# Optimization experiments

Hardware: AMD Instinct MI355X
Metric: run time of the kernel (lower is better)

The kernel has to match this reference:

```python
import jax, jax.numpy as jnp
import numpy as np


def setup_inputs() -> dict:
    key = jax.random.key(0)
    k1, k2 = jax.random.split(key)
    N = 16777216  # 16M 2D points
    preds = jax.random.normal(k1, (N, 2), dtype=jnp.float32)
    targets = jax.random.normal(k2, (N, 2), dtype=jnp.float32)
    return {"preds": preds, "targets": targets}


def reference(preds, targets):
    # per-sample 2D euclidean distance, fused in one pass
    d = preds - targets                      # [N, 2]
    dist = jnp.sqrt(jnp.sum(d * d, axis=1))  # [N]
    n = dist.shape[0]
    # Faithful to torch: loss tensor starts as zeros(1) and distances are
    # cat'ed on, so mean is over n+1 elements (including a leading zero).
    loss = jnp.sum(dist) / jnp.asarray(n + 1, dist.dtype)
    return loss
```

## Files before the change

### kernel.cpp

```cpp
#include <hip/hip_runtime.h>


typedef float floatx4 __attribute__((ext_vector_type(4)));

#define NBLOCKS 4096
#define NTHREADS 256
#define UNROLL 8

__global__ __launch_bounds__(NTHREADS, 2)
void dist_partial_kernel(const floatx4* __restrict__ preds,
                         const floatx4* __restrict__ targets,
                         float* __restrict__ partials,
                         int n4) {
    const int tile_base = blockIdx.x * (UNROLL * NTHREADS) + threadIdx.x;

    float acc = 0.0f;

    if (tile_base + (UNROLL - 1) * NTHREADS < n4) {
        floatx4 p[UNROLL], t[UNROLL];
        #pragma unroll
        for (int k = 0; k < UNROLL; ++k)
            p[k] = __builtin_nontemporal_load(&preds[tile_base + k * NTHREADS]);
        #pragma unroll
        for (int k = 0; k < UNROLL; ++k)
            t[k] = __builtin_nontemporal_load(&targets[tile_base + k * NTHREADS]);
        asm volatile("" ::: "memory");
        #pragma unroll
        for (int k = 0; k < UNROLL; ++k) {
            float dx0 = p[k].x - t[k].x;
            float dy0 = p[k].y - t[k].y;
            float dx1 = p[k].z - t[k].z;
            float dy1 = p[k].w - t[k].w;
            acc += sqrtf(dx0 * dx0 + dy0 * dy0);
            acc += sqrtf(dx1 * dx1 + dy1 * dy1);
        }
    } else {
        for (int k = 0; k < UNROLL; ++k) {
            int i = tile_base + k * NTHREADS;
            if (i < n4) {
                floatx4 p = preds[i];
                floatx4 t = targets[i];
                float dx0 = p.x - t.x;
                float dy0 = p.y - t.y;
                float dx1 = p.z - t.z;
                float dy1 = p.w - t.w;
                acc += sqrtf(dx0 * dx0 + dy0 * dy0);
                acc += sqrtf(dx1 * dx1 + dy1 * dy1);
            }
        }
    }

    #pragma unroll
    for (int off = 32; off > 0; off >>= 1)
        acc += __shfl_down(acc, off, 64);

    __shared__ float wave_sums[NTHREADS / 64];
    int lane = threadIdx.x & 63;
    int wave = threadIdx.x >> 6;
    if (lane == 0) wave_sums[wave] = acc;
    __syncthreads();

    if (threadIdx.x == 0) {
        float s = 0.0f;
        #pragma unroll
        for (int w = 0; w < NTHREADS / 64; ++w) s += wave_sums[w];
        partials[blockIdx.x] = s;
    }
}

__global__ __launch_bounds__(1024)
void dist_final_kernel(const float* __restrict__ partials,
                       float* __restrict__ out,
                       int nblocks, float inv_np1) {
    int tid = threadIdx.x;
    float acc = 0.0f;
    for (int i = tid; i < nblocks; i += 1024) acc += partials[i];

    #pragma unroll
    for (int off = 32; off > 0; off >>= 1)
        acc += __shfl_down(acc, off, 64);

    __shared__ float wave_sums[16];
    int lane = tid & 63;
    int wave = tid >> 6;
    if (lane == 0) wave_sums[wave] = acc;
    __syncthreads();

    if (tid == 0) {
        float s = 0.0f;
        #pragma unroll
        for (int w = 0; w < 16; ++w) s += wave_sums[w];
        out[0] = s * inv_np1;
    }
}

extern "C" void kernel_launch(void* const* d_in, const int* in_sizes, int n_in,
                              void* d_out, int out_size, void* d_ws, size_t ws_size,
                              hipStream_t stream) {
    const floatx4* preds   = (const floatx4*)d_in[0];
    const floatx4* targets = (const floatx4*)d_in[1];
    float* partials = (float*)d_ws;
    float* out = (float*)d_out;

    int n_elems  = in_sizes[0];
    int n_points = n_elems / 2;
    int n4       = n_elems / 4;

    float inv_np1 = 1.0f / (float)(n_points + 1);

    dist_partial_kernel<<<NBLOCKS, NTHREADS, 0, stream>>>(preds, targets, partials, n4);
    dist_final_kernel<<<1, 1024, 0, stream>>>(partials, out, NBLOCKS, inv_np1);
}
```

Baseline: 249.6 us.

## Double-buffer loads across stages with fewer, larger blocks

Each block now processes 16 float4 per thread in four stages of four, prefetching the next stage's preds/targets into a second register buffer while computing the current one. Block count is halved to 2048 so each block covers twice the data, and the launch-bounds occupancy hint is raised to 4. The aim is to keep memory requests in flight continuously rather than issuing one burst and then stalling. The double buffering holds two stages of inputs in registers at once, so register pressure may limit occupancy, and the smaller grid may use the memory channels less evenly.

```diff
diff --git a/kernel.cpp b/kernel.cpp
--- a/kernel.cpp
+++ b/kernel.cpp
@@ -3,49 +3,69 @@
 
 typedef float floatx4 __attribute__((ext_vector_type(4)));
 
-#define NBLOCKS 4096
+#define NBLOCKS 2048
 #define NTHREADS 256
-#define UNROLL 8
+#define STAGE 4
+#define NSTAGES 4
 
-__global__ __launch_bounds__(NTHREADS, 2)
+__global__ __launch_bounds__(NTHREADS, 4)
 void dist_partial_kernel(const floatx4* __restrict__ preds,
                          const floatx4* __restrict__ targets,
                          float* __restrict__ partials,
                          int n4) {
-    const int tile_base = blockIdx.x * (UNROLL * NTHREADS) + threadIdx.x;
+    const int span = STAGE * NSTAGES * NTHREADS;
+    const int base = blockIdx.x * span + threadIdx.x;
 
     float acc = 0.0f;
 
-    if (tile_base + (UNROLL - 1) * NTHREADS < n4) {
-        floatx4 p[UNROLL], t[UNROLL];
+    if (base + span - NTHREADS < n4) {
+        floatx4 pa[STAGE], ta[STAGE];
+        floatx4 pb[STAGE], tb[STAGE];
+
         #pragma unroll
-        for (int k = 0; k < UNROLL; ++k)
-            p[k] = __builtin_nontemporal_load(&preds[tile_base + k * NTHREADS]);
+        for (int k = 0; k < STAGE; ++k) {
+            pa[k] = __builtin_nontemporal_load(&preds[base + k * NTHREADS]);
+            ta[k] = __builtin_nontemporal_load(&targets[base + k * NTHREADS]);
+        }
+
         #pragma unroll
-        for (int k = 0; k < UNROLL; ++k)
-            t[k] = __builtin_nontemporal_load(&targets[tile_base + k * NTHREADS]);
-        asm volatile("" ::: "memory");
-        #pragma unroll
-        for (int k = 0; k < UNROLL; ++k) {
-            float dx0 = p[k].x - t[k].x;
-            float dy0 = p[k].y - t[k].y;
-            float dx1 = p[k].z - t[k].z;
-            float dy1 = p[k].w - t[k].w;
-            acc += sqrtf(dx0 * dx0 + dy0 * dy0);
-            acc += sqrtf(dx1 * dx1 + dy1 * dy1);
+        for (int s = 0; s < NSTAGES; ++s) {
+            if (s + 1 < NSTAGES) {
+                const int nb = base + (s + 1) * STAGE * NTHREADS;
+                #pragma unroll
+                for (int k = 0; k < STAGE; ++k) {
+                    pb[k] = __builtin_nontemporal_load(&preds[nb + k * NTHREADS]);
+                    tb[k] = __builtin_nontemporal_load(&targets[nb + k * NTHREADS]);
+                }
+            }
+            #pragma unroll
+            for (int k = 0; k < STAGE; ++k) {
+                float dx0 = pa[k].x - ta[k].x;
+                float dy0 = pa[k].y - ta[k].y;
+                float dx1 = pa[k].z - ta[k].z;
+                float dy1 = pa[k].w - ta[k].w;
+                acc += sqrtf(dx0 * dx0 + dy0 * dy0);
+                acc += sqrtf(dx1 * dx1 + dy1 * dy1);
+            }
+            if (s + 1 < NSTAGES) {
+                #pragma unroll
+                for (int k = 0; k < STAGE; ++k) { pa[k] = pb[k]; ta[k] = tb[k]; }
+            }
         }
     } else {
-        for (int k = 0; k < UNROLL; ++k) {
-            int i = tile_base + k * NTHREADS;
-            if (i < n4) {
-                floatx4 p = preds[i];
-                floatx4 t = targets[i];
-                float dx0 = p.x - t.x;
-                float dy0 = p.y - t.y;
-                float dx1 = p.z - t.z;
-                float dy1 = p.w - t.w;
-                acc += sqrtf(dx0 * dx0 + dy0 * dy0);
-                acc += sqrtf(dx1 * dx1 + dy1 * dy1);
+        for (int s = 0; s < NSTAGES; ++s) {
+            for (int k = 0; k < STAGE; ++k) {
+                int i = base + (s * STAGE + k) * NTHREADS;
+                if (i < n4) {
+                    floatx4 p = preds[i];
+                    floatx4 t = targets[i];
+                    float dx0 = p.x - t.x;
+                    float dy0 = p.y - t.y;
+                    float dx1 = p.z - t.z;
+                    float dy1 = p.w - t.w;
+                    acc += sqrtf(dx0 * dx0 + dy0 * dy0);
+                    acc += sqrtf(dx1 * dx1 + dy1 * dy1);
+                }
             }
         }
     }
```

New measurement: 246.9 us. About the same (-1.1%).

## Stream inputs through per-wave LDS ring with async global-to-LDS loads

Applied to the files above, without the earlier changes.

Replaces the unrolled register loads with a per-wave four-deep ring buffer in LDS filled by direct global-to-LDS loads, using explicit vmcnt waits to overlap fetching future tiles with computing the current one. Each block now covers a larger span with half as many blocks, and occupancy hints rise. It also switches to the hardware fast sqrt builtin. The risks are LDS slot reuse without an explicit LDS-read wait, and extra LDS traffic on a purely bandwidth-bound stream.

```diff
diff --git a/kernel.cpp b/kernel.cpp
--- a/kernel.cpp
+++ b/kernel.cpp
@@ -3,49 +3,86 @@
 
 typedef float floatx4 __attribute__((ext_vector_type(4)));
 
-#define NBLOCKS 4096
-#define NTHREADS 256
-#define UNROLL 8
+#define NBLOCKS    2048
+#define NTHREADS   256
+#define NWAVES     (NTHREADS / 64)
+#define DEPTH      4
+#define WAVE_TILES 16
+#define SPAN       (NWAVES * WAVE_TILES * 64)
 
-__global__ __launch_bounds__(NTHREADS, 2)
+#define WAITV(N) asm volatile("s_waitcnt vmcnt(" #N ")" ::: "memory")
+
+typedef const __attribute__((address_space(1))) void gvoid;
+typedef __attribute__((address_space(3))) void lvoid;
+
+__global__ __launch_bounds__(NTHREADS, 4)
 void dist_partial_kernel(const floatx4* __restrict__ preds,
                          const floatx4* __restrict__ targets,
                          float* __restrict__ partials,
                          int n4) {
-    const int tile_base = blockIdx.x * (UNROLL * NTHREADS) + threadIdx.x;
+    __shared__ floatx4 lds_p[NWAVES][DEPTH][64];
+    __shared__ floatx4 lds_t[NWAVES][DEPTH][64];
+
+    const int wave = threadIdx.x >> 6;
+    const int lane = threadIdx.x & 63;
+    const int block_base = blockIdx.x * SPAN;
+    const int wbase = block_base + wave * (WAVE_TILES * 64) + lane;
 
     float acc = 0.0f;
 
-    if (tile_base + (UNROLL - 1) * NTHREADS < n4) {
-        floatx4 p[UNROLL], t[UNROLL];
+    if (block_base + SPAN <= n4) {
         #pragma unroll
-        for (int k = 0; k < UNROLL; ++k)
-            p[k] = __builtin_nontemporal_load(&preds[tile_base + k * NTHREADS]);
+        for (int t = 0; t < DEPTH; ++t) {
+            __builtin_amdgcn_global_load_lds((gvoid*)&preds[wbase + t * 64],
+                                             (lvoid*)&lds_p[wave][t][0], 16, 0, 0);
+            __builtin_amdgcn_global_load_lds((gvoid*)&targets[wbase + t * 64],
+                                             (lvoid*)&lds_t[wave][t][0], 16, 0, 0);
+        }
+
         #pragma unroll
-        for (int k = 0; k < UNROLL; ++k)
-            t[k] = __builtin_nontemporal_load(&targets[tile_base + k * NTHREADS]);
-        asm volatile("" ::: "memory");
-        #pragma unroll
-        for (int k = 0; k < UNROLL; ++k) {
-            float dx0 = p[k].x - t[k].x;
-            float dy0 = p[k].y - t[k].y;
-            float dx1 = p[k].z - t[k].z;
-            float dy1 = p[k].w - t[k].w;
-            acc += sqrtf(dx0 * dx0 + dy0 * dy0);
-            acc += sqrtf(dx1 * dx1 + dy1 * dy1);
+        for (int t = 0; t < WAVE_TILES; ++t) {
+            const int rem = WAVE_TILES - 1 - t;
+            const int w   = 2 * (rem < DEPTH - 1 ? rem : DEPTH - 1);
+            switch (w) {
+                case 6: WAITV(6); break;
+                case 4: WAITV(4); break;
+                case 2: WAITV(2); break;
+                default: WAITV(0); break;
+            }
+            __builtin_amdgcn_sched_barrier(0);
+
+            const int slot = t & (DEPTH - 1);
+            floatx4 p  = lds_p[wave][slot][lane];
+            floatx4 tt = lds_t[wave][slot][lane];
+
+            float dx0 = p.x - tt.x;
+            float dy0 = p.y - tt.y;
+            float dx1 = p.z - tt.z;
+            float dy1 = p.w - tt.w;
+            acc += __builtin_amdgcn_sqrtf(dx0 * dx0 + dy0 * dy0);
+            acc += __builtin_amdgcn_sqrtf(dx1 * dx1 + dy1 * dy1);
+
+            asm volatile("" ::: "memory");
+
+            if (t + DEPTH < WAVE_TILES) {
+                __builtin_amdgcn_global_load_lds((gvoid*)&preds[wbase + (t + DEPTH) * 64],
+                                                 (lvoid*)&lds_p[wave][slot][0], 16, 0, 0);
+                __builtin_amdgcn_global_load_lds((gvoid*)&targets[wbase + (t + DEPTH) * 64],
+                                                 (lvoid*)&lds_t[wave][slot][0], 16, 0, 0);
+            }
         }
     } else {
-        for (int k = 0; k < UNROLL; ++k) {
-            int i = tile_base + k * NTHREADS;
+        for (int t = 0; t < WAVE_TILES; ++t) {
+            int i = wbase + t * 64;
             if (i < n4) {
-                floatx4 p = preds[i];
-                floatx4 t = targets[i];
-                float dx0 = p.x - t.x;
-                float dy0 = p.y - t.y;
-                float dx1 = p.z - t.z;
-                float dy1 = p.w - t.w;
-                acc += sqrtf(dx0 * dx0 + dy0 * dy0);
-                acc += sqrtf(dx1 * dx1 + dy1 * dy1);
+                floatx4 p  = preds[i];
+                floatx4 tt = targets[i];
+                float dx0 = p.x - tt.x;
+                float dy0 = p.y - tt.y;
+                float dx1 = p.z - tt.z;
+                float dy1 = p.w - tt.w;
+                acc += __builtin_amdgcn_sqrtf(dx0 * dx0 + dy0 * dy0);
+                acc += __builtin_amdgcn_sqrtf(dx1 * dx1 + dy1 * dy1);
             }
         }
     }
@@ -54,16 +91,14 @@
     for (int off = 32; off > 0; off >>= 1)
         acc += __shfl_down(acc, off, 64);
 
-    __shared__ float wave_sums[NTHREADS / 64];
-    int lane = threadIdx.x & 63;
-    int wave = threadIdx.x >> 6;
+    __shared__ float wave_sums[NWAVES];
     if (lane == 0) wave_sums[wave] = acc;
     __syncthreads();
 
     if (threadIdx.x == 0) {
         float s = 0.0f;
         #pragma unroll
-        for (int w = 0; w < NTHREADS / 64; ++w) s += wave_sums[w];
+        for (int w = 0; w < NWAVES; ++w) s += wave_sums[w];
         partials[blockIdx.x] = s;
     }
 }
```

New measurement: 273.3 us. +9.5%, slower.
